# Performance work log

Hardware: AMD Instinct MI355X
Metric: run time of the kernel (lower is better)

The kernel has to match this reference:

```python
import jax, jax.numpy as jnp
import numpy as np

B, D, C = 1024, 128, 100000
EPS = 1e-12  # torch F.normalize eps


def setup_inputs() -> dict:
    key = jax.random.key(0)
    k1, k2, k3 = jax.random.split(key, 3)
    # scale so ||x||^2 ~ 1, keeping exp(-dist) in a representable range
    xs = jax.random.normal(k1, (B, D), dtype=jnp.float32) / np.sqrt(D)
    ys = jax.random.randint(k2, (B,), 0, C, dtype=jnp.int64)
    # xavier_uniform init of Embedding(C, D): U(-a, a), a = sqrt(6/(C+D))
    a = np.sqrt(6.0 / (C + D))
    proxies = jax.random.uniform(k3, (C, D), dtype=jnp.float32, minval=-a, maxval=a)
    return {"xs": xs, "ys": ys, "proxies": proxies}


def reference(xs, ys, proxies):
    # L2-normalize every proxy (original normalizes pos proxy over dim=0 of a 1-D
    # vector and neg proxies over dim=1 -- both are per-proxy L2 normalization).
    norm = jnp.linalg.norm(proxies, axis=1, keepdims=True)
    P = proxies / jnp.maximum(norm, EPS)                      # [C, D], unit rows
    x_sq = jnp.sum(xs * xs, axis=1, keepdims=True)            # [B, 1]
    d = x_sq + 1.0 - 2.0 * (xs @ P.T)                         # [B, C]
    e = jnp.exp(-d)                                           # [B, C]
    pos = jnp.take_along_axis(e, ys[:, None], axis=1)[:, 0]   # exp(-d[b, y_b])
    neg_sum = jnp.sum(e, axis=1) - pos                        # denominator excludes the positive
    return jnp.mean(-jnp.log(pos / neg_sum))
```

## Files before the change

kernel.cpp:

```cpp
#include <hip/hip_runtime.h>
#include <hip/hip_fp16.h>

#define B_N 1024
#define D_K 128
#define C_N 100000
#define CT_PER_CHUNK 5
#define CCHUNK (CT_PER_CHUNK * 32)
#define NCHUNK (C_N / CCHUNK)
#define BSPLIT 4
#define NBLK_MAIN (NCHUNK * BSPLIT)
#define NREP 64
#define NPROXY_BLK (C_N / 4)
#define EPSN 1e-12f

typedef _Float16 half8 __attribute__((ext_vector_type(8)));
typedef float floatx16 __attribute__((ext_vector_type(16)));

union U16 { uint4 u; half8 h; };

__device__ __forceinline__ unsigned int pack2h(float a, float b) {
    union { _Float16 h[2]; unsigned int u; } p;
    p.h[0] = (_Float16)a; p.h[1] = (_Float16)b;
    return p.u;
}

__global__ __launch_bounds__(256) void prep_kernel(
    const float* __restrict__ xs, const int* __restrict__ ys,
    const float* __restrict__ proxies,
    unsigned int* __restrict__ pfrag, unsigned int* __restrict__ xfrag,
    float* __restrict__ w, float* __restrict__ posd,
    float* __restrict__ negsumR)
{
    int tid = threadIdx.x, wave = tid >> 6, lane = tid & 63;
    int bx = blockIdx.x;
    int ks = lane >> 3, kh = (lane >> 2) & 1, jq = lane & 3;

    if (bx < NPROXY_BLK) {
        int c = bx * 4 + wave;
        const float2 pv = ((const float2*)(proxies + (size_t)c * D_K))[lane];
        float ss = pv.x * pv.x + pv.y * pv.y;
        #pragma unroll
        for (int m = 1; m < 64; m <<= 1) ss += __shfl_xor(ss, m, 64);
        float sc = 1.0f / fmaxf(sqrtf(ss), EPSN);
        int idx = (((c >> 5) * 8 + ks) * 64 + ((c & 31) | (kh << 5))) * 4 + jq;
        pfrag[idx] = pack2h(pv.x * sc, pv.y * sc);
    } else {
        int bb = bx - NPROXY_BLK;
        negsumR[bb * 256 + tid] = 0.0f;

        int b = bb * 4 + wave;
        const float2 xv = ((const float2*)(xs + (size_t)b * D_K))[lane];
        float ss = xv.x * xv.x + xv.y * xv.y;
        #pragma unroll
        for (int m = 1; m < 64; m <<= 1) ss += __shfl_xor(ss, m, 64);
        float xsq = ss;

        int idx = (((b >> 5) * 8 + ks) * 64 + ((b & 31) | (kh << 5))) * 4 + jq;
        xfrag[idx] = pack2h(2.0f * xv.x, 2.0f * xv.y);

        int y = ys[b];
        const float2 pv = ((const float2*)(proxies + (size_t)y * D_K))[lane];
        float dt = xv.x * pv.x + xv.y * pv.y;
        float pp = pv.x * pv.x + pv.y * pv.y;
        #pragma unroll
        for (int m = 1; m < 64; m <<= 1) {
            dt += __shfl_xor(dt, m, 64);
            pp += __shfl_xor(pp, m, 64);
        }
        if (lane == 0) {
            w[b] = __expf(-xsq - 1.0f);
            float nrm = fmaxf(sqrtf(pp), EPSN);
            posd[b] = xsq + 1.0f - 2.0f * (dt / nrm);
        }
    }
}

__global__ __launch_bounds__(256, 3) void main_kernel(
    const uint4* __restrict__ pfrag, const uint4* __restrict__ xfrag,
    const float* __restrict__ w, float* __restrict__ negsumR)
{
    __shared__ uint4 ldsP[CT_PER_CHUNK * 8 * 64];

    int tid = threadIdx.x, wave = tid >> 6, lane = tid & 63;
    int bx = blockIdx.x;
    int cchunk = bx >> 2;
    int bs = bx & 3;

    {
        const uint4* src = pfrag + (size_t)cchunk * (CT_PER_CHUNK * 8 * 64);
        #pragma unroll
        for (int i = 0; i < 10; ++i) {
            int f = wave * 10 + i;
            __builtin_amdgcn_global_load_lds(
                (const __attribute__((address_space(1))) void*)(src + f * 64 + lane),
                (__attribute__((address_space(3))) void*)(ldsP + f * 64),
                16, 0, 0);
        }
    }

    int nt0 = bs * 8 + wave * 2;
    uint4 xf0[8], xf1[8];
    #pragma unroll
    for (int k = 0; k < 8; ++k) xf0[k] = xfrag[((nt0    ) * 8 + k) * 64 + lane];
    #pragma unroll
    for (int k = 0; k < 8; ++k) xf1[k] = xfrag[((nt0 + 1) * 8 + k) * 64 + lane];

    __syncthreads();

    float s0 = 0.0f, s1 = 0.0f;

    #pragma unroll 1
    for (int ct = 0; ct < CT_PER_CHUNK; ++ct) {
        uint4 a[8];
        #pragma unroll
        for (int k = 0; k < 8; ++k)
            a[k] = ldsP[(ct * 8 + k) * 64 + lane];

        floatx16 acc0, acc1;
        #pragma unroll
        for (int i = 0; i < 16; ++i) { acc0[i] = 0.0f; acc1[i] = 0.0f; }

        #pragma unroll
        for (int k = 0; k < 8; ++k) {
            U16 ua, u0, u1;
            ua.u = a[k]; u0.u = xf0[k]; u1.u = xf1[k];
            acc0 = __builtin_amdgcn_mfma_f32_32x32x16_f16(ua.h, u0.h, acc0, 0, 0, 0);
            acc1 = __builtin_amdgcn_mfma_f32_32x32x16_f16(ua.h, u1.h, acc1, 0, 0, 0);
        }

        #pragma unroll
        for (int i = 0; i < 16; ++i) {
            s0 += __expf(acc0[i]);
            s1 += __expf(acc1[i]);
        }
    }

    s0 += __shfl_xor(s0, 32, 64);
    s1 += __shfl_xor(s1, 32, 64);

    int rep = bx & (NREP - 1);
    if (lane < 32) {
        int b0 = bs * 256 + wave * 64 + lane;
        int b1 = b0 + 32;
        atomicAdd(&negsumR[rep * B_N + b0], s0 * w[b0]);
        atomicAdd(&negsumR[rep * B_N + b1], s1 * w[b1]);
    }
}

__global__ __launch_bounds__(1024) void final_kernel(
    const float* __restrict__ negsumR, const float* __restrict__ posd,
    float* __restrict__ out)
{
    __shared__ float red[1024];
    int t = threadIdx.x;
    float ns = 0.0f;
    #pragma unroll 4
    for (int r = 0; r < NREP; ++r) ns += negsumR[r * B_N + t];
    float pd = posd[t];
    red[t] = logf(ns - __expf(-pd)) + pd;
    __syncthreads();
    #pragma unroll
    for (int s = 512; s > 0; s >>= 1) {
        if (t < s) red[t] += red[t + s];
        __syncthreads();
    }
    if (t == 0) out[0] = red[0] * (1.0f / 1024.0f);
}

extern "C" void kernel_launch(void* const* d_in, const int* in_sizes, int n_in,
                              void* d_out, int out_size, void* d_ws, size_t ws_size,
                              hipStream_t stream)
{
    const float* xs      = (const float*)d_in[0];
    const int*   ys      = (const int*)d_in[1];
    const float* proxies = (const float*)d_in[2];

    char* ws = (char*)d_ws;
    unsigned int* pfrag   = (unsigned int*)ws;
    unsigned int* xfrag   = (unsigned int*)(ws + 25600000);
    float*        w       = (float*)(ws + 25600000 + 262144);
    float*        posd    = (float*)(ws + 25600000 + 262144 + 4096);
    float*        negsumR = (float*)(ws + 25600000 + 262144 + 8192);

    prep_kernel<<<NPROXY_BLK + 256, 256, 0, stream>>>(
        xs, ys, proxies, pfrag, xfrag, w, posd, negsumR);
    main_kernel<<<NBLK_MAIN, 256, 0, stream>>>(
        (const uint4*)pfrag, (const uint4*)xfrag, w, negsumR);
    final_kernel<<<1, 1024, 0, stream>>>(negsumR, posd, (float*)d_out);
}
```

Baseline: 137.1 us.

## Vectorize proxy prep and double batch tiles per main block

The proxy normalization now uses 8 threads per proxy row, with float4 loads and 16-byte fragment stores, in place of one wave per row with 4-byte scattered stores. Each main block now covers 4 batch tiles per wave in two passes over the same LDS proxy chunk, which halves the block count and the number of times each proxy chunk is loaded from global memory. The exp accumulation is split into two partial sums to give more instruction-level parallelism. The cost is less parallelism (fewer blocks) and serial work inside each block.

New measurement: 130.8 us. 1.05x faster.

```diff
diff --git a/kernel.cpp b/kernel.cpp
--- a/kernel.cpp
+++ b/kernel.cpp
@@ -7,10 +7,10 @@
 #define CT_PER_CHUNK 5
 #define CCHUNK (CT_PER_CHUNK * 32)
 #define NCHUNK (C_N / CCHUNK)
-#define BSPLIT 4
+#define BSPLIT 2
 #define NBLK_MAIN (NCHUNK * BSPLIT)
 #define NREP 64
-#define NPROXY_BLK (C_N / 4)
+#define NPROXY_BLK (C_N / 32)
 #define EPSN 1e-12f
 
 typedef _Float16 half8 __attribute__((ext_vector_type(8)));
@@ -27,27 +27,45 @@
 __global__ __launch_bounds__(256) void prep_kernel(
     const float* __restrict__ xs, const int* __restrict__ ys,
     const float* __restrict__ proxies,
-    unsigned int* __restrict__ pfrag, unsigned int* __restrict__ xfrag,
+    uint4* __restrict__ pfrag, unsigned int* __restrict__ xfrag,
     float* __restrict__ w, float* __restrict__ posd,
     float* __restrict__ negsumR)
 {
-    int tid = threadIdx.x, wave = tid >> 6, lane = tid & 63;
-    int bx = blockIdx.x;
-    int ks = lane >> 3, kh = (lane >> 2) & 1, jq = lane & 3;
+    int tid = threadIdx.x, bx = blockIdx.x;
 
     if (bx < NPROXY_BLK) {
-        int c = bx * 4 + wave;
-        const float2 pv = ((const float2*)(proxies + (size_t)c * D_K))[lane];
-        float ss = pv.x * pv.x + pv.y * pv.y;
-        #pragma unroll
-        for (int m = 1; m < 64; m <<= 1) ss += __shfl_xor(ss, m, 64);
+        int L = tid & 7;
+        int r = tid >> 3;
+        int c = bx * 32 + r;
+        const float4* src = (const float4*)(proxies + (size_t)c * D_K + L * 16);
+        float4 v0 = src[0], v1 = src[1], v2 = src[2], v3 = src[3];
+        float ss = v0.x*v0.x + v0.y*v0.y + v0.z*v0.z + v0.w*v0.w
+                 + v1.x*v1.x + v1.y*v1.y + v1.z*v1.z + v1.w*v1.w
+                 + v2.x*v2.x + v2.y*v2.y + v2.z*v2.z + v2.w*v2.w
+                 + v3.x*v3.x + v3.y*v3.y + v3.z*v3.z + v3.w*v3.w;
+        ss += __shfl_xor(ss, 1, 64);
+        ss += __shfl_xor(ss, 2, 64);
+        ss += __shfl_xor(ss, 4, 64);
         float sc = 1.0f / fmaxf(sqrtf(ss), EPSN);
-        int idx = (((c >> 5) * 8 + ks) * 64 + ((c & 31) | (kh << 5))) * 4 + jq;
-        pfrag[idx] = pack2h(pv.x * sc, pv.y * sc);
+
+        union { _Float16 h[8]; uint4 u; } pa, pb;
+        pa.h[0]=(_Float16)(v0.x*sc); pa.h[1]=(_Float16)(v0.y*sc);
+        pa.h[2]=(_Float16)(v0.z*sc); pa.h[3]=(_Float16)(v0.w*sc);
+        pa.h[4]=(_Float16)(v1.x*sc); pa.h[5]=(_Float16)(v1.y*sc);
+        pa.h[6]=(_Float16)(v1.z*sc); pa.h[7]=(_Float16)(v1.w*sc);
+        pb.h[0]=(_Float16)(v2.x*sc); pb.h[1]=(_Float16)(v2.y*sc);
+        pb.h[2]=(_Float16)(v2.z*sc); pb.h[3]=(_Float16)(v2.w*sc);
+        pb.h[4]=(_Float16)(v3.x*sc); pb.h[5]=(_Float16)(v3.y*sc);
+        pb.h[6]=(_Float16)(v3.z*sc); pb.h[7]=(_Float16)(v3.w*sc);
+
+        uint4* dst = pfrag + (size_t)bx * 512;
+        dst[L * 64 + r]      = pa.u;
+        dst[L * 64 + 32 + r] = pb.u;
     } else {
         int bb = bx - NPROXY_BLK;
         negsumR[bb * 256 + tid] = 0.0f;
 
+        int wave = tid >> 6, lane = tid & 63;
         int b = bb * 4 + wave;
         const float2 xv = ((const float2*)(xs + (size_t)b * D_K))[lane];
         float ss = xv.x * xv.x + xv.y * xv.y;
@@ -55,6 +73,7 @@
         for (int m = 1; m < 64; m <<= 1) ss += __shfl_xor(ss, m, 64);
         float xsq = ss;
 
+        int ks = lane >> 3, kh = (lane >> 2) & 1, jq = lane & 3;
         int idx = (((b >> 5) * 8 + ks) * 64 + ((b & 31) | (kh << 5))) * 4 + jq;
         xfrag[idx] = pack2h(2.0f * xv.x, 2.0f * xv.y);
 
@@ -75,6 +94,41 @@
     }
 }
 
+__device__ __forceinline__ void compute_pair(
+    const uint4* ldsP, int lane,
+    const uint4 xfA[8], const uint4 xfB[8],
+    float& outA, float& outB)
+{
+    float sA0 = 0.f, sA1 = 0.f, sB0 = 0.f, sB1 = 0.f;
+    #pragma unroll 1
+    for (int ct = 0; ct < CT_PER_CHUNK; ++ct) {
+        uint4 a[8];
+        #pragma unroll
+        for (int k = 0; k < 8; ++k)
+            a[k] = ldsP[(ct * 8 + k) * 64 + lane];
+
+        floatx16 accA, accB;
+        #pragma unroll
+        for (int i = 0; i < 16; ++i) { accA[i] = 0.0f; accB[i] = 0.0f; }
+
+        #pragma unroll
+        for (int k = 0; k < 8; ++k) {
+            U16 ua, u0, u1;
+            ua.u = a[k]; u0.u = xfA[k]; u1.u = xfB[k];
+            accA = __builtin_amdgcn_mfma_f32_32x32x16_f16(ua.h, u0.h, accA, 0, 0, 0);
+            accB = __builtin_amdgcn_mfma_f32_32x32x16_f16(ua.h, u1.h, accB, 0, 0, 0);
+        }
+
+        #pragma unroll
+        for (int i = 0; i < 16; i += 2) {
+            sA0 += __expf(accA[i]);     sA1 += __expf(accA[i + 1]);
+            sB0 += __expf(accB[i]);     sB1 += __expf(accB[i + 1]);
+        }
+    }
+    outA = sA0 + sA1;
+    outB = sB0 + sB1;
+}
+
 __global__ __launch_bounds__(256, 3) void main_kernel(
     const uint4* __restrict__ pfrag, const uint4* __restrict__ xfrag,
     const float* __restrict__ w, float* __restrict__ negsumR)
@@ -83,8 +137,8 @@
 
     int tid = threadIdx.x, wave = tid >> 6, lane = tid & 63;
     int bx = blockIdx.x;
-    int cchunk = bx >> 2;
-    int bs = bx & 3;
+    int cchunk = bx >> 1;
+    int bs = bx & 1;
 
     {
         const uint4* src = pfrag + (size_t)cchunk * (CT_PER_CHUNK * 8 * 64);
@@ -98,52 +152,44 @@
         }
     }
 
-    int nt0 = bs * 8 + wave * 2;
-    uint4 xf0[8], xf1[8];
-    #pragma unroll
-    for (int k = 0; k < 8; ++k) xf0[k] = xfrag[((nt0    ) * 8 + k) * 64 + lane];
-    #pragma unroll
-    for (int k = 0; k < 8; ++k) xf1[k] = xfrag[((nt0 + 1) * 8 + k) * 64 + lane];
+    int nt0 = bs * 16 + wave * 4;
+    uint4 xfA[8], xfB[8];
+    #pragma unroll
+    for (int k = 0; k < 8; ++k) xfA[k] = xfrag[((nt0    ) * 8 + k) * 64 + lane];
+    #pragma unroll
+    for (int k = 0; k < 8; ++k) xfB[k] = xfrag[((nt0 + 1) * 8 + k) * 64 + lane];
 
     __syncthreads();
 
-    float s0 = 0.0f, s1 = 0.0f;
-
-    #pragma unroll 1
-    for (int ct = 0; ct < CT_PER_CHUNK; ++ct) {
-        uint4 a[8];
-        #pragma unroll
-        for (int k = 0; k < 8; ++k)
-            a[k] = ldsP[(ct * 8 + k) * 64 + lane];
-
-        floatx16 acc0, acc1;
-        #pragma unroll
-        for (int i = 0; i < 16; ++i) { acc0[i] = 0.0f; acc1[i] = 0.0f; }
-
-        #pragma unroll
-        for (int k = 0; k < 8; ++k) {
-            U16 ua, u0, u1;
-            ua.u = a[k]; u0.u = xf0[k]; u1.u = xf1[k];
-            acc0 = __builtin_amdgcn_mfma_f32_32x32x16_f16(ua.h, u0.h, acc0, 0, 0, 0);
-            acc1 = __builtin_amdgcn_mfma_f32_32x32x16_f16(ua.h, u1.h, acc1, 0, 0, 0);
-        }
-
-        #pragma unroll
-        for (int i = 0; i < 16; ++i) {
-            s0 += __expf(acc0[i]);
-            s1 += __expf(acc1[i]);
-        }
-    }
+    int rep = bx & (NREP - 1);
+    float* nsr = negsumR + (size_t)rep * B_N;
+
+    float s0, s1;
+    compute_pair(ldsP, lane, xfA, xfB, s0, s1);
+
+    #pragma unroll
+    for (int k = 0; k < 8; ++k) xfA[k] = xfrag[((nt0 + 2) * 8 + k) * 64 + lane];
+    #pragma unroll
+    for (int k = 0; k < 8; ++k) xfB[k] = xfrag[((nt0 + 3) * 8 + k) * 64 + lane];
 
     s0 += __shfl_xor(s0, 32, 64);
     s1 += __shfl_xor(s1, 32, 64);
-
-    int rep = bx & (NREP - 1);
     if (lane < 32) {
-        int b0 = bs * 256 + wave * 64 + lane;
-        int b1 = b0 + 32;
-        atomicAdd(&negsumR[rep * B_N + b0], s0 * w[b0]);
-        atomicAdd(&negsumR[rep * B_N + b1], s1 * w[b1]);
+        int b0 = (nt0    ) * 32 + lane;
+        int b1 = (nt0 + 1) * 32 + lane;
+        atomicAdd(&nsr[b0], s0 * w[b0]);
+        atomicAdd(&nsr[b1], s1 * w[b1]);
+    }
+
+    float s2, s3;
+    compute_pair(ldsP, lane, xfA, xfB, s2, s3);
+    s2 += __shfl_xor(s2, 32, 64);
+    s3 += __shfl_xor(s3, 32, 64);
+    if (lane < 32) {
+        int b2 = (nt0 + 2) * 32 + lane;
+        int b3 = (nt0 + 3) * 32 + lane;
+        atomicAdd(&nsr[b2], s2 * w[b2]);
+        atomicAdd(&nsr[b3], s3 * w[b3]);
     }
 }
 
@@ -176,7 +222,7 @@
     const float* proxies = (const float*)d_in[2];
 
     char* ws = (char*)d_ws;
-    unsigned int* pfrag   = (unsigned int*)ws;
+    uint4*        pfrag   = (uint4*)ws;
     unsigned int* xfrag   = (unsigned int*)(ws + 25600000);
     float*        w       = (float*)(ws + 25600000 + 262144);
     float*        posd    = (float*)(ws + 25600000 + 262144 + 4096);
@@ -185,6 +231,6 @@
     prep_kernel<<<NPROXY_BLK + 256, 256, 0, stream>>>(
         xs, ys, proxies, pfrag, xfrag, w, posd, negsumR);
     main_kernel<<<NBLK_MAIN, 256, 0, stream>>>(
-        (const uint4*)pfrag, (const uint4*)xfrag, w, negsumR);
+        pfrag, (const uint4*)xfrag, w, negsumR);
     final_kernel<<<1, 1024, 0, stream>>>(negsumR, posd, (float*)d_out);
 }
```
